# Performance work log

Hardware: AMD Instinct MI355X
Metric: run time of the kernel (lower is better)

## Reference

```python
import jax, jax.numpy as jnp
import numpy as np

B, C, H, W = 4, 256, 64, 64
C8 = C // 8


def setup_inputs() -> dict:
    key = jax.random.key(0)
    ks = jax.random.split(key, 8)
    x = jax.random.normal(ks[0], (B, C, H, W), dtype=jnp.float32)
    # 1x1 conv weights act as per-pixel linear maps: [out_ch, in_ch]
    Wq = jax.random.normal(ks[1], (C8, C), dtype=jnp.float32) * 0.05
    bq = jax.random.normal(ks[2], (C8,), dtype=jnp.float32) * 0.01
    Wk = jax.random.normal(ks[3], (C8, C), dtype=jnp.float32) * 0.05
    bk = jax.random.normal(ks[4], (C8,), dtype=jnp.float32) * 0.01
    Wv = jax.random.normal(ks[5], (C, C), dtype=jnp.float32) * 0.05
    bv = jax.random.normal(ks[6], (C,), dtype=jnp.float32) * 0.01
    # torch inits gamma to 0 (identity); use nonzero so output exercises the attention path
    gamma = jnp.array(0.5, dtype=jnp.float32)
    return {"x": x, "Wq": Wq, "bq": bq, "Wk": Wk, "bk": bk, "Wv": Wv, "bv": bv, "gamma": gamma}


def reference(x, Wq, bq, Wk, bk, Wv, bv, gamma):
    b, c, h, w = x.shape
    n = h * w
    xf = x.reshape(b, c, n)                                   # [B,C,N]
    q = jnp.einsum('oc,bcn->bno', Wq, xf) + bq                # [B,N,C8] (proj_query permuted)
    k = jnp.einsum('oc,bcn->bon', Wk, xf) + bk[:, None]       # [B,C8,N]
    energy = jnp.einsum('bnc,bcm->bnm', q, k)                 # [B,N_q,N_k]
    # NOTE: torch Softmax(dim=1) -> normalize over the QUERY axis (axis=1)
    attention = jax.nn.softmax(energy, axis=1)
    v = jnp.einsum('oc,bcn->bon', Wv, xf) + bv[:, None]       # [B,C,N]
    out = jnp.einsum('bcn,bnm->bcm', v, attention).reshape(b, c, h, w)
    return gamma * out + x
```

## Files before the change

kernel.cpp:

```cpp
#include <hip/hip_runtime.h>
#include <hip/hip_bf16.h>

#define BN 4
#define CC 256
#define C8 32
#define NN 4096
#define PROJ_ROWS 320

typedef __attribute__((ext_vector_type(8))) short short8;
typedef __attribute__((ext_vector_type(4))) float f32x4;
typedef __attribute__((ext_vector_type(4))) unsigned short u16x4;

__device__ __forceinline__ unsigned short f2bf(float f) {
    unsigned u = __builtin_bit_cast(unsigned, f);
    unsigned r = (u + 0x7fffu + ((u >> 16) & 1u)) >> 16;
    return (unsigned short)r;
}

__device__ __forceinline__ float bf2f(unsigned short s) {
    return __builtin_bit_cast(float, ((unsigned)s) << 16);
}

#define GL16(gsrc, ldst)                                                     \
    __builtin_amdgcn_global_load_lds(                                        \
        (const __attribute__((address_space(1))) void*)(gsrc),               \
        (__attribute__((address_space(3))) void*)(ldst), 16, 0, 0)

__global__ __launch_bounds__(64) void prep_kernel(
    const float* __restrict__ Wq, const float* __restrict__ Wk,
    const float* __restrict__ Wv, unsigned short* __restrict__ Wb)
{
    int row = blockIdx.x;
    int l = threadIdx.x;
    const float* src = (row < 32) ? (Wq + (size_t)row * CC)
                     : (row < 64) ? (Wk + (size_t)(row - 32) * CC)
                                  : (Wv + (size_t)(row - 64) * CC);
    float4 v = *(const float4*)(src + l * 4);
    unsigned short t4[4] __attribute__((aligned(8)))
        = {f2bf(v.x), f2bf(v.y), f2bf(v.z), f2bf(v.w)};
    *(u16x4*)(Wb + (size_t)row * CC + l * 4) =
        (u16x4){t4[0], t4[1], t4[2], t4[3]};
}

__global__ __launch_bounds__(256) void proj_kernel(
    const float* __restrict__ x, const unsigned short* __restrict__ Wb,
    const float* __restrict__ bq, const float* __restrict__ bk,
    const float* __restrict__ bv,
    unsigned short* __restrict__ proj, unsigned short* __restrict__ qT)
{
    int bid = blockIdx.x;
    int b = bid >> 7, nt = bid & 127;
    int n0 = nt * 32;
    int tid = threadIdx.x;
    int w = tid >> 6, l = tid & 63, l15 = l & 15, lq = l >> 4;

    __shared__ alignas(16) unsigned short Xt[32][264];

    int c_l = tid >> 3;
    int nb  = (tid & 7) * 4;

#pragma unroll
    for (int kc = 0; kc < 8; kc++) {
        const float* xp = x + ((size_t)(b * CC + kc * 32 + c_l)) * NN + n0 + nb;
        float4 x0 = *(const float4*)xp;
        float t[4] = {x0.x, x0.y, x0.z, x0.w};
#pragma unroll
        for (int e = 0; e < 4; e++) Xt[nb + e][kc * 32 + c_l] = f2bf(t[e]);
    }
    __syncthreads();

    f32x4 acc[5][2];
#pragma unroll
    for (int gi = 0; gi < 5; gi++)
#pragma unroll
        for (int mi = 0; mi < 2; mi++) acc[gi][mi] = (f32x4){0.f, 0.f, 0.f, 0.f};

    for (int kc = 0; kc < 8; kc++) {
#pragma unroll
        for (int gi = 0; gi < 5; gi++) {
            int og = (w * 5 + gi) * 16 + l15;
            short8 af = *(const short8*)(Wb + (size_t)og * CC + kc * 32 + lq * 8);
#pragma unroll
            for (int mi = 0; mi < 2; mi++) {
                short8 bf = *(const short8*)&Xt[mi * 16 + l15][kc * 32 + lq * 8];
                acc[gi][mi] = __builtin_amdgcn_mfma_f32_16x16x32_bf16(af, bf, acc[gi][mi], 0, 0, 0);
            }
        }
    }

#pragma unroll
    for (int gi = 0; gi < 5; gi++) {
#pragma unroll
        for (int r = 0; r < 4; r++) {
            int og = (w * 5 + gi) * 16 + lq * 4 + r;
            float bias = (og < 32) ? bq[og] : (og < 64) ? bk[og - 32] : bv[og - 64];
#pragma unroll
            for (int mi = 0; mi < 2; mi++) {
                int n = n0 + mi * 16 + l15;
                unsigned short v16 = f2bf(acc[gi][mi][r] + bias);
                if (og < 32) {
                    qT[((size_t)b * NN + n) * C8 + og] = v16;
                } else {
                    proj[((size_t)b * PROJ_ROWS + og) * NN + n] = v16;
                }
            }
        }
    }
}

template<int NSPLIT, bool FINAL>
__global__ __launch_bounds__(1024, 4) void attn_kernel(
    const unsigned short* __restrict__ proj,
    const unsigned short* __restrict__ qT,
    const float* __restrict__ x,
    const float* __restrict__ gamma_p,
    float* __restrict__ out,
    unsigned short* __restrict__ Opart,
    float* __restrict__ Lpart)
{
    constexpr int ITERS = 64 / NSPLIT;
    constexpr int LOGN  = (NSPLIT == 4) ? 2 : (NSPLIT == 2) ? 1 : 0;
    int bid = blockIdx.x;
    int xcd = bid & 7;
    int b   = xcd >> 1;
    int h   = (bid >> 3) & (NSPLIT - 1);
    int mt  = ((bid >> (3 + LOGN)) << 1) | (xcd & 1);
    int m0  = mt * 256;
    int nbase = h * (ITERS * 64);

    int tid = threadIdx.x;
    int w = tid >> 6, l = tid & 63, l15 = l & 15, lq = l >> 4;
    int wc = w & 3;
    int wm = w >> 2;

    __shared__ alignas(16) unsigned short vlds[2][256 * 64];
    __shared__ alignas(16) unsigned short qlds[2][2048];
    __shared__ alignas(16) unsigned short ps[2][256][72];
    __shared__ float red[4][256];
    __shared__ float Ltot[256];

    const unsigned short* kbase = proj + ((size_t)b * PROJ_ROWS + C8) * NN;
    const unsigned short* vbase = proj + ((size_t)b * PROJ_ROWS + 64) * NN;
    const unsigned short* qbase = qT + (size_t)b * NN * C8;

    short8 kfrag[4];
#pragma unroll
    for (int mi = 0; mi < 4; mi++) {
        int col = m0 + 64 * wm + mi * 16 + l15;
        unsigned short t8[8] __attribute__((aligned(16)));
#pragma unroll
        for (int j = 0; j < 8; j++)
            t8[j] = kbase[(size_t)(lq * 8 + j) * NN + col];
        kfrag[mi] = *(const short8*)t8;
    }

    int vc_sub = l >> 3;
    int vjsw   = (l & 7) ^ (l >> 3);

    auto stageV = [&](int buf, int t) {
        int n0s = nbase + t * 64;
#pragma unroll
        for (int r = 0; r < 2; r++) {
            int crow = (r * 16 + w) * 8 + vc_sub;
            const unsigned short* src = vbase + (size_t)crow * NN + n0s + vjsw * 8;
            GL16(src, &vlds[buf][(r * 16 + w) * 512]);
        }
    };
    auto stageQ = [&](int buf, int t) {
        if (w < 4) {
            const unsigned short* src = qbase + (size_t)(nbase + t * 64) * C8 + (w * 64 + l) * 8;
            GL16(src, &qlds[buf][w * 512]);
        }
    };

    f32x4 O[4][4];
#pragma unroll
    for (int ci = 0; ci < 4; ci++)
#pragma unroll
        for (int mi = 0; mi < 4; mi++) O[ci][mi] = (f32x4){0.f, 0.f, 0.f, 0.f};
    float runS[4] = {0.f, 0.f, 0.f, 0.f};

    auto S_phase = [&](int pb, int qb) {
        short8 qfrag = *(const short8*)&qlds[qb][(16 * wc + l15) * 32 + lq * 8];
#pragma unroll
        for (int mi = 0; mi < 4; mi++) {
            f32x4 S = __builtin_amdgcn_mfma_f32_16x16x32_bf16(
                qfrag, kfrag[mi], (f32x4){0.f, 0.f, 0.f, 0.f}, 0, 0, 0);
            float p0 = __expf(S[0]);
            float p1 = __expf(S[1]);
            float p2 = __expf(S[2]);
            float p3 = __expf(S[3]);
            runS[mi] += (p0 + p1) + (p2 + p3);
            unsigned pk0 = (unsigned)f2bf(p0) | ((unsigned)f2bf(p1) << 16);
            unsigned pk1 = (unsigned)f2bf(p2) | ((unsigned)f2bf(p3) << 16);
            *(uint2*)&ps[pb][64 * wm + mi * 16 + l15][16 * wc + lq * 4]
                = make_uint2(pk0, pk1);
        }
    };

    stageV(0, 0);
    stageQ(0, 0);
    if (ITERS > 1) stageQ(1, 1);
    __syncthreads();
    S_phase(0, 0);

    for (int it = 0; it < ITERS; it++) {
        __syncthreads();

        if (it + 1 < ITERS) stageV((it + 1) & 1, it + 1);
        if (it + 2 < ITERS) stageQ((it + 2) & 1, it + 2);

        int vb = it & 1;
#pragma unroll
        for (int kh = 0; kh < 2; kh++) {
            short8 av[4];
#pragma unroll
            for (int ci = 0; ci < 4; ci++) {
                int c = 64 * wc + ci * 16 + l15;
                av[ci] = *(const short8*)&vlds[vb][c * 64 + (((kh * 4 + lq) ^ (c & 7)) * 8)];
            }
            short8 bfr[4];
#pragma unroll
            for (int mi = 0; mi < 4; mi++)
                bfr[mi] = *(const short8*)&ps[vb][64 * wm + mi * 16 + l15][kh * 32 + lq * 8];
#pragma unroll
            for (int ci = 0; ci < 4; ci++)
#pragma unroll
                for (int mi = 0; mi < 4; mi++)
                    O[ci][mi] = __builtin_amdgcn_mfma_f32_16x16x32_bf16(
                        av[ci], bfr[mi], O[ci][mi], 0, 0, 0);
        }

        if (it + 1 < ITERS) S_phase((it + 1) & 1, (it + 1) & 1);
    }

#pragma unroll
    for (int mi = 0; mi < 4; mi++) {
        float s2 = runS[mi];
        s2 += __shfl_xor(s2, 16);
        s2 += __shfl_xor(s2, 32);
        red[wc][64 * wm + mi * 16 + l15] = s2;
    }
    __syncthreads();

    if constexpr (FINAL) {
        if (tid < 256) Ltot[tid] = red[0][tid] + red[1][tid] + red[2][tid] + red[3][tid];
        __syncthreads();
        float gamma = gamma_p[0];
        float iv[4];
#pragma unroll
        for (int mi = 0; mi < 4; mi++) iv[mi] = 1.0f / Ltot[64 * wm + mi * 16 + l15];
#pragma unroll
        for (int ci = 0; ci < 4; ci++) {
#pragma unroll
            for (int mi = 0; mi < 4; mi++) {
                int m = m0 + 64 * wm + mi * 16 + l15;
#pragma unroll
                for (int r = 0; r < 4; r++) {
                    int c = 64 * wc + ci * 16 + lq * 4 + r;
                    size_t idx = ((size_t)b * CC + c) * NN + m;
                    out[idx] = gamma * (O[ci][mi][r] * iv[mi]) + x[idx];
                }
            }
        }
    } else {
        size_t p = ((size_t)h * BN + b) * 16 + mt;
        if (tid < 256)
            Lpart[p * 256 + tid] = red[0][tid] + red[1][tid] + red[2][tid] + red[3][tid];
        unsigned short* Ob = Opart + p * (size_t)(CC * 256);
#pragma unroll
        for (int ci = 0; ci < 4; ci++) {
#pragma unroll
            for (int mi = 0; mi < 4; mi++) {
#pragma unroll
                for (int r = 0; r < 4; r++) {
                    int c = 64 * wc + ci * 16 + lq * 4 + r;
                    int m = 64 * wm + mi * 16 + l15;
                    Ob[(size_t)c * 256 + m] = f2bf(O[ci][mi][r]);
                }
            }
        }
    }
}

template<int NSPLIT>
__global__ __launch_bounds__(256) void combine_kernel(
    const unsigned short* __restrict__ Opart, const float* __restrict__ Lpart,
    const float* __restrict__ x, const float* __restrict__ gamma_p,
    float* __restrict__ out)
{
    int bid = blockIdx.x;
    int cq = bid & 31;
    int mt = (bid >> 5) & 15;
    int b  = bid >> 9;
    int tid = threadIdx.x;
    int m4 = (tid & 63) * 4;
    int ci4 = tid >> 6;
    float gamma = gamma_p[0];

    f32x4 Ls = (f32x4){0.f, 0.f, 0.f, 0.f};
#pragma unroll
    for (int h = 0; h < NSPLIT; h++) {
        size_t p = ((size_t)h * BN + b) * 16 + mt;
        Ls += *(const f32x4*)(Lpart + p * 256 + m4);
    }
    f32x4 inv;
#pragma unroll
    for (int j = 0; j < 4; j++) inv[j] = 1.0f / Ls[j];

#pragma unroll
    for (int cp = 0; cp < 2; cp++) {
        int c = cq * 8 + cp * 4 + ci4;
        f32x4 acc = (f32x4){0.f, 0.f, 0.f, 0.f};
#pragma unroll
        for (int h = 0; h < NSPLIT; h++) {
            size_t p = ((size_t)h * BN + b) * 16 + mt;
            u16x4 o4 = *(const u16x4*)(Opart + p * (size_t)(CC * 256) + (size_t)c * 256 + m4);
#pragma unroll
            for (int j = 0; j < 4; j++) acc[j] += bf2f(o4[j]);
        }
        size_t idx = ((size_t)b * CC + c) * NN + mt * 256 + m4;
        f32x4 xv = *(const f32x4*)(x + idx);
        f32x4 o;
#pragma unroll
        for (int j = 0; j < 4; j++) o[j] = gamma * (acc[j] * inv[j]) + xv[j];
        *(f32x4*)(out + idx) = o;
    }
}

extern "C" void kernel_launch(void* const* d_in, const int* in_sizes, int n_in,
                              void* d_out, int out_size, void* d_ws, size_t ws_size,
                              hipStream_t stream) {
    const float* x     = (const float*)d_in[0];
    const float* Wq    = (const float*)d_in[1];
    const float* bq    = (const float*)d_in[2];
    const float* Wk    = (const float*)d_in[3];
    const float* bk    = (const float*)d_in[4];
    const float* Wv    = (const float*)d_in[5];
    const float* bv    = (const float*)d_in[6];
    const float* gamma = (const float*)d_in[7];
    float* out = (float*)d_out;
    (void)in_sizes; (void)n_in; (void)out_size;

    unsigned short* proj = (unsigned short*)d_ws;
    unsigned short* qT   = proj + (size_t)BN * PROJ_ROWS * NN;
    unsigned short* Wb   = qT + (size_t)BN * NN * C8;
    const size_t baseB = ((size_t)BN * PROJ_ROWS * NN + (size_t)BN * NN * C8) * 2
                       + (size_t)PROJ_ROWS * CC * 2;

    auto needB = [&](int ns) {
        size_t LpB = (size_t)ns * BN * 16 * 256 * 4;
        size_t OpB = (size_t)ns * BN * 16 * CC * 256 * 2;
        return baseB + LpB + OpB;
    };

    prep_kernel<<<320, 64, 0, stream>>>(Wq, Wk, Wv, Wb);
    proj_kernel<<<512, 256, 0, stream>>>(x, Wb, bq, bk, bv, proj, qT);

    if (ws_size >= needB(4)) {
        float* Lpart = (float*)((char*)d_ws + baseB);
        unsigned short* Opart = (unsigned short*)(Lpart + (size_t)4 * BN * 16 * 256);
        attn_kernel<4, false><<<256, 1024, 0, stream>>>(proj, qT, x, gamma, out, Opart, Lpart);
        combine_kernel<4><<<2048, 256, 0, stream>>>(Opart, Lpart, x, gamma, out);
    } else if (ws_size >= needB(2)) {
        float* Lpart = (float*)((char*)d_ws + baseB);
        unsigned short* Opart = (unsigned short*)(Lpart + (size_t)2 * BN * 16 * 256);
        attn_kernel<2, false><<<128, 1024, 0, stream>>>(proj, qT, x, gamma, out, Opart, Lpart);
        combine_kernel<2><<<2048, 256, 0, stream>>>(Opart, Lpart, x, gamma, out);
    } else {
        attn_kernel<1, true><<<64, 1024, 0, stream>>>(proj, qT, x, gamma, out, nullptr, nullptr);
    }
}
```

Measured before the change: 164.9 us.

## Fuse projection, attention and combine into one cooperative kernel with grid syncs

Replaces the proj, attn and combine launches with a single cooperative kernel of 256 blocks. Grid-wide syncs separate the three phases, and each block re-maps its work per phase. This removes two kernel launches and the gaps between them. In exchange the projection and combine phases run on only 256 blocks instead of 512 and 2048, which may reduce parallelism, and each grid.sync adds its own barrier cost.

Result: slower. 529.9 us (+221.3%).

```diff
diff --git a/kernel.cpp b/kernel.cpp
--- a/kernel.cpp
+++ b/kernel.cpp
@@ -1,5 +1,8 @@
 #include <hip/hip_runtime.h>
 #include <hip/hip_bf16.h>
+#include <hip/hip_cooperative_groups.h>
+
+namespace cg = cooperative_groups;
 
 #define BN 4
 #define CC 256
@@ -40,6 +43,263 @@
         = {f2bf(v.x), f2bf(v.y), f2bf(v.z), f2bf(v.w)};
     *(u16x4*)(Wb + (size_t)row * CC + l * 4) =
         (u16x4){t4[0], t4[1], t4[2], t4[3]};
+}
+
+__global__ __launch_bounds__(1024, 4) void fused_kernel(
+    const float* __restrict__ x, const unsigned short* __restrict__ Wb,
+    const float* __restrict__ bq, const float* __restrict__ bk,
+    const float* __restrict__ bv, const float* __restrict__ gamma_p,
+    float* __restrict__ out,
+    unsigned short* __restrict__ proj, unsigned short* __restrict__ qT,
+    unsigned short* __restrict__ Opart, float* __restrict__ Lpart)
+{
+    constexpr int NSPLIT = 4;
+    constexpr int ITERS = 64 / NSPLIT;
+    int bid = blockIdx.x;
+    int xcd = bid & 7;
+    int b   = xcd >> 1;
+
+    int tid = threadIdx.x;
+    int w = tid >> 6, l = tid & 63, l15 = l & 15, lq = l >> 4;
+
+    __shared__ alignas(16) unsigned short vlds[2][256 * 64];
+    __shared__ alignas(16) unsigned short qlds[2][2048];
+    __shared__ alignas(16) unsigned short ps[2][256][72];
+    __shared__ float red[4][256];
+    __shared__ float Ltot[256];
+
+    cg::grid_group grid = cg::this_grid();
+
+    {
+        int nt = ((bid >> 3) & 31) | ((xcd & 1) << 5);
+        int n0 = nt * 64;
+
+        unsigned short (*Xt)[264] = reinterpret_cast<unsigned short(*)[264]>(&vlds[0][0]);
+
+        {
+            int c = tid >> 2, nb = (tid & 3) * 16;
+            const float* xp = x + ((size_t)(b * CC + c)) * NN + n0 + nb;
+#pragma unroll
+            for (int q4 = 0; q4 < 4; q4++) {
+                float4 x0 = *(const float4*)(xp + q4 * 4);
+                float t[4] = {x0.x, x0.y, x0.z, x0.w};
+#pragma unroll
+                for (int e = 0; e < 4; e++) Xt[nb + q4 * 4 + e][c] = f2bf(t[e]);
+            }
+        }
+        __syncthreads();
+
+        int ng = (w < 4) ? 2 : 1;
+        f32x4 acc[2][4];
+#pragma unroll
+        for (int s = 0; s < 2; s++)
+#pragma unroll
+            for (int mi = 0; mi < 4; mi++) acc[s][mi] = (f32x4){0.f, 0.f, 0.f, 0.f};
+
+        for (int s = 0; s < ng; s++) {
+            int g = (s == 0) ? w : 16 + w;
+            int og = g * 16 + l15;
+            for (int kc = 0; kc < 8; kc++) {
+                short8 af = *(const short8*)(Wb + (size_t)og * CC + kc * 32 + lq * 8);
+#pragma unroll
+                for (int mi = 0; mi < 4; mi++) {
+                    short8 bf = *(const short8*)&Xt[mi * 16 + l15][kc * 32 + lq * 8];
+                    acc[s][mi] = __builtin_amdgcn_mfma_f32_16x16x32_bf16(af, bf, acc[s][mi], 0, 0, 0);
+                }
+            }
+        }
+
+        for (int s = 0; s < ng; s++) {
+            int g = (s == 0) ? w : 16 + w;
+#pragma unroll
+            for (int r = 0; r < 4; r++) {
+                int og = g * 16 + lq * 4 + r;
+                float bias = (og < 32) ? bq[og] : (og < 64) ? bk[og - 32] : bv[og - 64];
+#pragma unroll
+                for (int mi = 0; mi < 4; mi++) {
+                    int n = n0 + mi * 16 + l15;
+                    unsigned short v16 = f2bf(acc[s][mi][r] + bias);
+                    if (og < 32) {
+                        qT[((size_t)b * NN + n) * C8 + og] = v16;
+                    } else {
+                        proj[((size_t)b * PROJ_ROWS + og) * NN + n] = v16;
+                    }
+                }
+            }
+        }
+    }
+
+    __threadfence();
+    grid.sync();
+
+    {
+        int h   = (bid >> 3) & (NSPLIT - 1);
+        int mt  = ((bid >> 5) << 1) | (xcd & 1);
+        int m0  = mt * 256;
+        int nbase = h * (ITERS * 64);
+        int wc = w & 3, wm = w >> 2;
+
+        const unsigned short* kbase = proj + ((size_t)b * PROJ_ROWS + C8) * NN;
+        const unsigned short* vbase = proj + ((size_t)b * PROJ_ROWS + 64) * NN;
+        const unsigned short* qbase = qT + (size_t)b * NN * C8;
+
+        short8 kfrag[4];
+#pragma unroll
+        for (int mi = 0; mi < 4; mi++) {
+            int col = m0 + 64 * wm + mi * 16 + l15;
+            unsigned short t8[8] __attribute__((aligned(16)));
+#pragma unroll
+            for (int j = 0; j < 8; j++)
+                t8[j] = kbase[(size_t)(lq * 8 + j) * NN + col];
+            kfrag[mi] = *(const short8*)t8;
+        }
+
+        int vc_sub = l >> 3;
+        int vjsw   = (l & 7) ^ (l >> 3);
+
+        auto stageV = [&](int buf, int t) {
+            int n0s = nbase + t * 64;
+#pragma unroll
+            for (int r = 0; r < 2; r++) {
+                int crow = (r * 16 + w) * 8 + vc_sub;
+                const unsigned short* src = vbase + (size_t)crow * NN + n0s + vjsw * 8;
+                GL16(src, &vlds[buf][(r * 16 + w) * 512]);
+            }
+        };
+        auto stageQ = [&](int buf, int t) {
+            if (w < 4) {
+                const unsigned short* src = qbase + (size_t)(nbase + t * 64) * C8 + (w * 64 + l) * 8;
+                GL16(src, &qlds[buf][w * 512]);
+            }
+        };
+
+        f32x4 O[4][4];
+#pragma unroll
+        for (int ci = 0; ci < 4; ci++)
+#pragma unroll
+            for (int mi = 0; mi < 4; mi++) O[ci][mi] = (f32x4){0.f, 0.f, 0.f, 0.f};
+        float runS[4] = {0.f, 0.f, 0.f, 0.f};
+
+        auto S_phase = [&](int pb, int qb) {
+            short8 qfrag = *(const short8*)&qlds[qb][(16 * wc + l15) * 32 + lq * 8];
+#pragma unroll
+            for (int mi = 0; mi < 4; mi++) {
+                f32x4 S = __builtin_amdgcn_mfma_f32_16x16x32_bf16(
+                    qfrag, kfrag[mi], (f32x4){0.f, 0.f, 0.f, 0.f}, 0, 0, 0);
+                float p0 = __expf(S[0]);
+                float p1 = __expf(S[1]);
+                float p2 = __expf(S[2]);
+                float p3 = __expf(S[3]);
+                runS[mi] += (p0 + p1) + (p2 + p3);
+                unsigned pk0 = (unsigned)f2bf(p0) | ((unsigned)f2bf(p1) << 16);
+                unsigned pk1 = (unsigned)f2bf(p2) | ((unsigned)f2bf(p3) << 16);
+                *(uint2*)&ps[pb][64 * wm + mi * 16 + l15][16 * wc + lq * 4]
+                    = make_uint2(pk0, pk1);
+            }
+        };
+
+        stageV(0, 0);
+        stageQ(0, 0);
+        stageQ(1, 1);
+        __syncthreads();
+        S_phase(0, 0);
+
+        for (int it = 0; it < ITERS; it++) {
+            __syncthreads();
+
+            if (it + 1 < ITERS) stageV((it + 1) & 1, it + 1);
+            if (it + 2 < ITERS) stageQ((it + 2) & 1, it + 2);
+
+            int vb = it & 1;
+#pragma unroll
+            for (int kh = 0; kh < 2; kh++) {
+                short8 av[4];
+#pragma unroll
+                for (int ci = 0; ci < 4; ci++) {
+                    int c = 64 * wc + ci * 16 + l15;
+                    av[ci] = *(const short8*)&vlds[vb][c * 64 + (((kh * 4 + lq) ^ (c & 7)) * 8)];
+                }
+                short8 bfr[4];
+#pragma unroll
+                for (int mi = 0; mi < 4; mi++)
+                    bfr[mi] = *(const short8*)&ps[vb][64 * wm + mi * 16 + l15][kh * 32 + lq * 8];
+#pragma unroll
+                for (int ci = 0; ci < 4; ci++)
+#pragma unroll
+                    for (int mi = 0; mi < 4; mi++)
+                        O[ci][mi] = __builtin_amdgcn_mfma_f32_16x16x32_bf16(
+                            av[ci], bfr[mi], O[ci][mi], 0, 0, 0);
+            }
+
+            if (it + 1 < ITERS) S_phase((it + 1) & 1, (it + 1) & 1);
+        }
+
+#pragma unroll
+        for (int mi = 0; mi < 4; mi++) {
+            float s2 = runS[mi];
+            s2 += __shfl_xor(s2, 16);
+            s2 += __shfl_xor(s2, 32);
+            red[wc][64 * wm + mi * 16 + l15] = s2;
+        }
+        __syncthreads();
+
+        size_t p = ((size_t)h * BN + b) * 16 + mt;
+        if (tid < 256)
+            Lpart[p * 256 + tid] = red[0][tid] + red[1][tid] + red[2][tid] + red[3][tid];
+        unsigned short* Ob = Opart + p * (size_t)(CC * 256);
+#pragma unroll
+        for (int ci = 0; ci < 4; ci++) {
+#pragma unroll
+            for (int mi = 0; mi < 4; mi++) {
+#pragma unroll
+                for (int r = 0; r < 4; r++) {
+                    int c = 64 * wc + ci * 16 + lq * 4 + r;
+                    int m = 64 * wm + mi * 16 + l15;
+                    Ob[(size_t)c * 256 + m] = f2bf(O[ci][mi][r]);
+                }
+            }
+        }
+    }
+
+    __threadfence();
+    grid.sync();
+
+    {
+        int sub = ((bid >> 3) & 31) | ((xcd & 1) << 5);
+        int mt2 = sub >> 2;
+        int cq  = sub & 3;
+        int m4 = (tid & 63) * 4;
+        float gamma = gamma_p[0];
+
+        f32x4 Ls = (f32x4){0.f, 0.f, 0.f, 0.f};
+#pragma unroll
+        for (int h = 0; h < NSPLIT; h++) {
+            size_t p = ((size_t)h * BN + b) * 16 + mt2;
+            Ls += *(const f32x4*)(Lpart + p * 256 + m4);
+        }
+        f32x4 inv;
+#pragma unroll
+        for (int j = 0; j < 4; j++) inv[j] = 1.0f / Ls[j];
+
+#pragma unroll
+        for (int j = 0; j < 4; j++) {
+            int c = cq * 64 + j * 16 + w;
+            f32x4 acc = (f32x4){0.f, 0.f, 0.f, 0.f};
+#pragma unroll
+            for (int h = 0; h < NSPLIT; h++) {
+                size_t p = ((size_t)h * BN + b) * 16 + mt2;
+                u16x4 o4 = *(const u16x4*)(Opart + p * (size_t)(CC * 256) + (size_t)c * 256 + m4);
+#pragma unroll
+                for (int e = 0; e < 4; e++) acc[e] += bf2f(o4[e]);
+            }
+            size_t idx = ((size_t)b * CC + c) * NN + mt2 * 256 + m4;
+            f32x4 xv = *(const f32x4*)(x + idx);
+            f32x4 o;
+#pragma unroll
+            for (int e = 0; e < 4; e++) o[e] = gamma * (acc[e] * inv[e]) + xv[e];
+            *(f32x4*)(out + idx) = o;
+        }
+    }
 }
 
 __global__ __launch_bounds__(256) void proj_kernel(
@@ -130,8 +390,7 @@
 
     int tid = threadIdx.x;
     int w = tid >> 6, l = tid & 63, l15 = l & 15, lq = l >> 4;
-    int wc = w & 3;
-    int wm = w >> 2;
+    int wc = w & 3, wm = w >> 2;
 
     __shared__ alignas(16) unsigned short vlds[2][256 * 64];
     __shared__ alignas(16) unsigned short qlds[2][2048];
@@ -355,19 +614,23 @@
     };
 
     prep_kernel<<<320, 64, 0, stream>>>(Wq, Wk, Wv, Wb);
-    proj_kernel<<<512, 256, 0, stream>>>(x, Wb, bq, bk, bv, proj, qT);
 
     if (ws_size >= needB(4)) {
         float* Lpart = (float*)((char*)d_ws + baseB);
         unsigned short* Opart = (unsigned short*)(Lpart + (size_t)4 * BN * 16 * 256);
-        attn_kernel<4, false><<<256, 1024, 0, stream>>>(proj, qT, x, gamma, out, Opart, Lpart);
-        combine_kernel<4><<<2048, 256, 0, stream>>>(Opart, Lpart, x, gamma, out);
+        void* args[] = {(void*)&x, (void*)&Wb, (void*)&bq, (void*)&bk, (void*)&bv,
+                        (void*)&gamma, (void*)&out, (void*)&proj, (void*)&qT,
+                        (void*)&Opart, (void*)&Lpart};
+        hipLaunchCooperativeKernel((void*)fused_kernel, dim3(256), dim3(1024),
+                                   args, 0, stream);
     } else if (ws_size >= needB(2)) {
         float* Lpart = (float*)((char*)d_ws + baseB);
         unsigned short* Opart = (unsigned short*)(Lpart + (size_t)2 * BN * 16 * 256);
+        proj_kernel<<<512, 256, 0, stream>>>(x, Wb, bq, bk, bv, proj, qT);
         attn_kernel<2, false><<<128, 1024, 0, stream>>>(proj, qT, x, gamma, out, Opart, Lpart);
         combine_kernel<2><<<2048, 256, 0, stream>>>(Opart, Lpart, x, gamma, out);
     } else {
+        proj_kernel<<<512, 256, 0, stream>>>(x, Wb, bq, bk, bv, proj, qT);
         attn_kernel<1, true><<<64, 1024, 0, stream>>>(proj, qT, x, gamma, out, nullptr, nullptr);
     }
 }
```

## Fuse split-K combine into attention kernel via last-block atomic counter

Applied to the files above, without the earlier changes.

Removes the separate combine kernel launch. Each attention block now bumps a per-(batch, m-tile) atomic counter after writing its partial O and L. The last-arriving block then reduces all splits, normalizes, applies gamma, adds the residual and writes the output. This saves a kernel launch and the idle gap between kernels, but serializes the combine work onto 64 blocks and adds a memset plus fences.

Measured after the change: 204.6 us. 1.24x slower.

```diff
diff --git a/kernel.cpp b/kernel.cpp
--- a/kernel.cpp
+++ b/kernel.cpp
@@ -116,7 +116,8 @@
     const float* __restrict__ gamma_p,
     float* __restrict__ out,
     unsigned short* __restrict__ Opart,
-    float* __restrict__ Lpart)
+    float* __restrict__ Lpart,
+    int* __restrict__ flags)
 {
     constexpr int ITERS = 64 / NSPLIT;
     constexpr int LOGN  = (NSPLIT == 4) ? 2 : (NSPLIT == 2) ? 1 : 0;
@@ -138,6 +139,7 @@
     __shared__ alignas(16) unsigned short ps[2][256][72];
     __shared__ float red[4][256];
     __shared__ float Ltot[256];
+    __shared__ int lastFlag;
 
     const unsigned short* kbase = proj + ((size_t)b * PROJ_ROWS + C8) * NN;
     const unsigned short* vbase = proj + ((size_t)b * PROJ_ROWS + 64) * NN;
@@ -280,51 +282,46 @@
                 }
             }
         }
-    }
-}
-
-template<int NSPLIT>
-__global__ __launch_bounds__(256) void combine_kernel(
-    const unsigned short* __restrict__ Opart, const float* __restrict__ Lpart,
-    const float* __restrict__ x, const float* __restrict__ gamma_p,
-    float* __restrict__ out)
-{
-    int bid = blockIdx.x;
-    int cq = bid & 31;
-    int mt = (bid >> 5) & 15;
-    int b  = bid >> 9;
-    int tid = threadIdx.x;
-    int m4 = (tid & 63) * 4;
-    int ci4 = tid >> 6;
-    float gamma = gamma_p[0];
-
-    f32x4 Ls = (f32x4){0.f, 0.f, 0.f, 0.f};
-#pragma unroll
-    for (int h = 0; h < NSPLIT; h++) {
-        size_t p = ((size_t)h * BN + b) * 16 + mt;
-        Ls += *(const f32x4*)(Lpart + p * 256 + m4);
-    }
-    f32x4 inv;
-#pragma unroll
-    for (int j = 0; j < 4; j++) inv[j] = 1.0f / Ls[j];
-
-#pragma unroll
-    for (int cp = 0; cp < 2; cp++) {
-        int c = cq * 8 + cp * 4 + ci4;
-        f32x4 acc = (f32x4){0.f, 0.f, 0.f, 0.f};
-#pragma unroll
-        for (int h = 0; h < NSPLIT; h++) {
-            size_t p = ((size_t)h * BN + b) * 16 + mt;
-            u16x4 o4 = *(const u16x4*)(Opart + p * (size_t)(CC * 256) + (size_t)c * 256 + m4);
-#pragma unroll
-            for (int j = 0; j < 4; j++) acc[j] += bf2f(o4[j]);
-        }
-        size_t idx = ((size_t)b * CC + c) * NN + mt * 256 + m4;
-        f32x4 xv = *(const f32x4*)(x + idx);
-        f32x4 o;
-#pragma unroll
-        for (int j = 0; j < 4; j++) o[j] = gamma * (acc[j] * inv[j]) + xv[j];
-        *(f32x4*)(out + idx) = o;
+
+        __syncthreads();
+        if (tid == 0) {
+            __threadfence();
+            lastFlag = (atomicAdd(&flags[b * 16 + mt], 1) == NSPLIT - 1) ? 1 : 0;
+        }
+        __syncthreads();
+        if (lastFlag) {
+            __threadfence();
+            float gamma = gamma_p[0];
+            int m4 = (tid & 63) * 4;
+            int cgrp = tid >> 6;
+
+            f32x4 Ls = (f32x4){0.f, 0.f, 0.f, 0.f};
+#pragma unroll
+            for (int h2 = 0; h2 < NSPLIT; h2++)
+                Ls += *(const f32x4*)(Lpart + (((size_t)h2 * BN + b) * 16 + mt) * 256 + m4);
+            f32x4 inv;
+#pragma unroll
+            for (int j = 0; j < 4; j++) inv[j] = 1.0f / Ls[j];
+
+            for (int cp = 0; cp < 16; cp++) {
+                int c = cp * 16 + cgrp;
+                f32x4 acc = (f32x4){0.f, 0.f, 0.f, 0.f};
+#pragma unroll
+                for (int h2 = 0; h2 < NSPLIT; h2++) {
+                    size_t p2 = ((size_t)h2 * BN + b) * 16 + mt;
+                    u16x4 o4 = *(const u16x4*)(Opart + p2 * (size_t)(CC * 256)
+                                               + (size_t)c * 256 + m4);
+#pragma unroll
+                    for (int j = 0; j < 4; j++) acc[j] += bf2f(o4[j]);
+                }
+                size_t idx = ((size_t)b * CC + c) * NN + mt * 256 + m4;
+                f32x4 xv = *(const f32x4*)(x + idx);
+                f32x4 o;
+#pragma unroll
+                for (int j = 0; j < 4; j++) o[j] = gamma * (acc[j] * inv[j]) + xv[j];
+                *(f32x4*)(out + idx) = o;
+            }
+        }
     }
 }
 
@@ -351,7 +348,7 @@
     auto needB = [&](int ns) {
         size_t LpB = (size_t)ns * BN * 16 * 256 * 4;
         size_t OpB = (size_t)ns * BN * 16 * CC * 256 * 2;
-        return baseB + LpB + OpB;
+        return baseB + LpB + OpB + 64 * sizeof(int);
     };
 
     prep_kernel<<<320, 64, 0, stream>>>(Wq, Wk, Wv, Wb);
@@ -360,14 +357,19 @@
     if (ws_size >= needB(4)) {
         float* Lpart = (float*)((char*)d_ws + baseB);
         unsigned short* Opart = (unsigned short*)(Lpart + (size_t)4 * BN * 16 * 256);
-        attn_kernel<4, false><<<256, 1024, 0, stream>>>(proj, qT, x, gamma, out, Opart, Lpart);
-        combine_kernel<4><<<2048, 256, 0, stream>>>(Opart, Lpart, x, gamma, out);
+        int* flags = (int*)(Opart + (size_t)4 * BN * 16 * CC * 256);
+        hipMemsetAsync(flags, 0, 64 * sizeof(int), stream);
+        attn_kernel<4, false><<<256, 1024, 0, stream>>>(proj, qT, x, gamma, out,
+                                                        Opart, Lpart, flags);
     } else if (ws_size >= needB(2)) {
         float* Lpart = (float*)((char*)d_ws + baseB);
         unsigned short* Opart = (unsigned short*)(Lpart + (size_t)2 * BN * 16 * 256);
-        attn_kernel<2, false><<<128, 1024, 0, stream>>>(proj, qT, x, gamma, out, Opart, Lpart);
-        combine_kernel<2><<<2048, 256, 0, stream>>>(Opart, Lpart, x, gamma, out);
+        int* flags = (int*)(Opart + (size_t)2 * BN * 16 * CC * 256);
+        hipMemsetAsync(flags, 0, 64 * sizeof(int), stream);
+        attn_kernel<2, false><<<128, 1024, 0, stream>>>(proj, qT, x, gamma, out,
+                                                        Opart, Lpart, flags);
     } else {
-        attn_kernel<1, true><<<64, 1024, 0, stream>>>(proj, qT, x, gamma, out, nullptr, nullptr);
-    }
-}
+        attn_kernel<1, true><<<64, 1024, 0, stream>>>(proj, qT, x, gamma, out,
+                                                      nullptr, nullptr, nullptr);
+    }
+}
```
